# Kernel optimization log

Hardware: AMD Instinct MI355X
Metric: run time of the kernel (lower is better)

Reference implementation:

```python
import jax, jax.numpy as jnp
import numpy as np

B, N, K, EMB, OUT = 16, 1024, 20, 1024, 40
EPS = 1e-5  # BatchNorm eps; eval mode with running_mean=0, running_var=1


def _bn(x, g, b):
    # inference-mode batchnorm (running_mean=0, running_var=1) over channel axis 1
    shp = [1] * x.ndim
    shp[1] = x.shape[1]
    inv = 1.0 / jnp.sqrt(1.0 + EPS)
    return x * inv * g.reshape(shp) + b.reshape(shp)


def _lrelu(v):
    return jnp.where(v >= 0, v, 0.2 * v)


def _knn(x, k):
    # x: (B, C, N) -> (B, N, k) indices of k nearest neighbours
    inner = -2.0 * jnp.einsum('bcn,bcm->bnm', x, x)
    xx = jnp.sum(x * x, axis=1)  # (B, N)
    pd = -xx[:, :, None] - inner - xx[:, None, :]  # negative squared distance
    return jax.lax.top_k(pd, k)[1]


def _graph_feature(x, k):
    # x: (B, C, N) -> (B, 2C, N, k) edge features [x_j - x_i, x_i]
    idx = _knn(x, k)                          # (B, N, k)
    xt = jnp.transpose(x, (0, 2, 1))          # (B, N, C)
    feat = jax.vmap(lambda pts, ind: pts[ind])(xt, idx)  # (B, N, k, C)
    ctr = xt[:, :, None, :]                   # (B, N, 1, C)
    out = jnp.concatenate([feat - ctr, jnp.broadcast_to(ctr, feat.shape)], axis=3)
    return jnp.transpose(out, (0, 3, 1, 2))   # (B, 2C, N, k)


def _local_frames(x, k):
    # x: (B, 3, N) -> (B, 6, N, k); eigh-based local frame + topk gather (no_grad in torch)
    B_, _, N_ = x.shape
    diff = jnp.transpose(x[:, :, None, :] - x[:, :, :, None], (0, 2, 1, 3))  # (B,N,3,N): y[b,i,c,j]=x[b,c,j]-x[b,c,i]
    cov = jnp.einsum('bncm,bndm->bncd', diff, diff)  # (B,N,3,3)
    _, vecs = jnp.linalg.eigh(cov)
    y = jnp.einsum('bndc,bndm->bncm', vecs, diff)    # eigvecs^T @ diff, (B,N,3,N)
    diag = jnp.transpose(jnp.diagonal(y, axis1=1, axis2=3), (0, 2, 1))  # (B,N,3) = y[b,n,:,n]
    y_sub = y - diag[:, :, :, None]
    red = jnp.sum(y_sub * y_sub, axis=2)             # (B,N,N)
    idx = jax.lax.top_k(red, k)[1]                   # (B,N,k) largest
    idxe = jnp.broadcast_to(idx[:, :, None, :], (B_, N_, 3, k))
    gy = jnp.take_along_axis(y, idxe, axis=3)
    gs = jnp.take_along_axis(y_sub, idxe, axis=3)
    x0 = jnp.concatenate([gy, gs], axis=2)           # (B,N,6,k)
    return jnp.transpose(x0, (0, 2, 1, 3))           # (B,6,N,k)


def setup_inputs() -> dict:
    key = jax.random.key(0)
    ks = jax.random.split(key, 30)
    rn = lambda k_, s, sc=0.05: jax.random.normal(k_, s, jnp.float32) * sc
    gm = lambda k_, c: 1.0 + 0.1 * jax.random.normal(k_, (c,), jnp.float32)
    bt = lambda k_, c: 0.1 * jax.random.normal(k_, (c,), jnp.float32)
    return {
        'x': jax.random.normal(ks[0], (B, 3, N), jnp.float32),
        'w1': rn(ks[1], (64, 6)),    'g1': gm(ks[2], 64),  'b1': bt(ks[3], 64),
        'w2': rn(ks[4], (64, 128)),  'g2': gm(ks[5], 64),  'b2': bt(ks[6], 64),
        'w3': rn(ks[7], (128, 128)), 'g3': gm(ks[8], 128), 'b3': bt(ks[9], 128),
        'w4': rn(ks[10], (256, 256)),'g4': gm(ks[11], 256),'b4': bt(ks[12], 256),
        'w5': rn(ks[13], (EMB, 512)),'g5': gm(ks[14], EMB),'b5': bt(ks[15], EMB),
        'lw1': rn(ks[16], (512, 2 * EMB)), 'g6': gm(ks[17], 512), 'b6': bt(ks[18], 512),
        'lw2': rn(ks[19], (256, 512)), 'lb2': bt(ks[20], 256), 'g7': gm(ks[21], 256), 'b7': bt(ks[22], 256),
        'lw3': rn(ks[23], (OUT, 256)), 'lb3': bt(ks[24], OUT),
    }


def reference(x, w1, g1, b1, w2, g2, b2, w3, g3, b3, w4, g4, b4,
              w5, g5, b5, lw1, g6, b6, lw2, lb2, g7, b7, lw3, lb3):
    x0 = jax.lax.stop_gradient(_local_frames(x, K))      # torch.no_grad block
    h = _lrelu(_bn(jnp.einsum('oc,bcnk->bonk', w1, x0), g1, b1))
    x1 = jnp.max(h, axis=-1)                              # (B,64,N)
    h = _lrelu(_bn(jnp.einsum('oc,bcnk->bonk', w2, _graph_feature(x1, K)), g2, b2))
    x2 = jnp.max(h, axis=-1)                              # (B,64,N)
    h = _lrelu(_bn(jnp.einsum('oc,bcnk->bonk', w3, _graph_feature(x2, K)), g3, b3))
    x3 = jnp.max(h, axis=-1)                              # (B,128,N)
    h = _lrelu(_bn(jnp.einsum('oc,bcnk->bonk', w4, _graph_feature(x3, K)), g4, b4))
    x4 = jnp.max(h, axis=-1)                              # (B,256,N)
    xc = jnp.concatenate([x1, x2, x3, x4], axis=1)        # (B,512,N)
    h5 = _lrelu(_bn(jnp.einsum('oc,bcn->bon', w5, xc), g5, b5))  # (B,EMB,N)
    f = jnp.concatenate([jnp.max(h5, axis=-1), jnp.mean(h5, axis=-1)], axis=1)  # (B,2*EMB)
    f = _lrelu(_bn(f @ lw1.T, g6, b6))                    # dropout = identity (eval)
    f = _lrelu(_bn(f @ lw2.T + lb2, g7, b7))
    return f @ lw3.T + lb3                                # (B,OUT)
```

## Files before the change

kernel.cpp:

```cpp
#include <hip/hip_runtime.h>
#include <hip/hip_bf16.h>
#include <math.h>

#define BB 16
#define NN 1024
#define KK 20


__device__ inline float s_sign(float a, float b) { return b >= 0.0f ? fabsf(a) : -fabsf(a); }

__device__ inline float s_lapy2(float x, float y) {
    float xa = fabsf(x), ya = fabsf(y);
    float w = fmaxf(xa, ya), z = fminf(xa, ya);
    if (z == 0.0f) return w;
    float t = z / w;
    return w * sqrtf(1.0f + t * t);
}

__device__ inline void s_lartg(float f, float g, float& c, float& s, float& r) {
    const float safmin = 1.1754943508222875e-38f;
    const float safmax = 1.0f / 1.1754943508222875e-38f;
    const float rtmin = 1.0842021724855044e-19f;
    const float rtmax = 9.2233720368547758e+18f;
    float f1 = fabsf(f), g1 = fabsf(g);
    if (g == 0.0f) { c = 1.0f; s = 0.0f; r = f; }
    else if (f == 0.0f) { c = 0.0f; s = (g >= 0.0f ? 1.0f : -1.0f); r = g1; }
    else {
        float d;
        if (f1 > rtmin && f1 < rtmax && g1 > rtmin && g1 < rtmax) {
            d = sqrtf(f * f + g * g);
            c = f1 / d;
            r = (f >= 0.0f ? d : -d);
        } else {
            float u = fminf(safmax, fmaxf(safmin, fmaxf(f1, g1)));
            float fs = f / u, gs = g / u;
            d = sqrtf(fs * fs + gs * gs);
            c = fabsf(fs) / d;
            r = (f >= 0.0f ? d : -d);
            r = r * u;
        }
        s = g / r;
    }
}

__device__ void s_laev2(float a, float b, float cc, float& rt1, float& rt2,
                        float& cs1, float& sn1) {
    float sm = a + cc;
    float df = a - cc;
    float adf = fabsf(df);
    float tb = b + b;
    float ab = fabsf(tb);
    float acmx, acmn;
    if (fabsf(a) > fabsf(cc)) { acmx = a; acmn = cc; } else { acmx = cc; acmn = a; }
    float rt;
    if (adf > ab) { float t = ab / adf; rt = adf * sqrtf(1.0f + t * t); }
    else if (adf < ab) { float t = adf / ab; rt = ab * sqrtf(1.0f + t * t); }
    else rt = ab * sqrtf(2.0f);
    int sgn1;
    if (sm < 0.0f) { rt1 = 0.5f * (sm - rt); sgn1 = -1; rt2 = (acmx / rt1) * acmn - (b / rt1) * b; }
    else if (sm > 0.0f) { rt1 = 0.5f * (sm + rt); sgn1 = 1; rt2 = (acmx / rt1) * acmn - (b / rt1) * b; }
    else { rt1 = 0.5f * rt; rt2 = -0.5f * rt; sgn1 = 1; }
    float cs; int sgn2;
    if (df >= 0.0f) { cs = df + rt; sgn2 = 1; } else { cs = df - rt; sgn2 = -1; }
    float acs = fabsf(cs);
    if (acs > ab) {
        float ct = -tb / cs;
        sn1 = 1.0f / sqrtf(1.0f + ct * ct);
        cs1 = ct * sn1;
    } else {
        if (ab == 0.0f) { cs1 = 1.0f; sn1 = 0.0f; }
        else {
            float tn = -cs / tb;
            cs1 = 1.0f / sqrtf(1.0f + tn * tn);
            sn1 = tn * cs1;
        }
    }
    if (sgn1 == sgn2) { float tn = cs1; cs1 = -sn1; sn1 = tn; }
}

__device__ void ssteqr3(float* d, float* e, float z[4][4]) {
    const float EPS = 5.9604644775390625e-08f;
    const float EPS2 = 3.5527136788005009e-15f;
    const float SAFMIN = 1.1754943508222875e-38f;
    const float SAFMAX = 1.0f / 1.1754943508222875e-38f;
    const float SSFMAX = sqrtf(SAFMAX) / 3.0f;
    const float SSFMIN = sqrtf(SAFMIN) / EPS2;
    const int n = 3;
    float cwork[4], swork[4];
    int nmaxit = n * 30, jtot = 0;
    int l1 = 1, nm1 = n - 1;
    int l, lsv, lend, lendsv, m, iscale;
    float anorm = 0.0f, p, g, r, c, s, f, b, rt1, rt2;
    int i, j, mm;
    float tst, sc, temp, ct, st;

L10:
    if (l1 > n) goto L160;
    if (l1 > 1) e[l1 - 1] = 0.0f;
    if (l1 <= nm1) {
        for (m = l1; m <= nm1; ++m) {
            tst = fabsf(e[m]);
            if (tst == 0.0f) goto L30;
            if (tst <= (sqrtf(fabsf(d[m])) * sqrtf(fabsf(d[m + 1]))) * EPS) { e[m] = 0.0f; goto L30; }
        }
    }
    m = n;
L30:
    l = l1; lsv = l; lend = m; lendsv = lend; l1 = m + 1;
    if (lend == l) goto L10;
    anorm = 0.0f;
    for (i = l; i <= lend; ++i) anorm = fmaxf(anorm, fabsf(d[i]));
    for (i = l; i <= lend - 1; ++i) anorm = fmaxf(anorm, fabsf(e[i]));
    iscale = 0;
    if (anorm == 0.0f) goto L10;
    if (anorm > SSFMAX) {
        iscale = 1; sc = SSFMAX / anorm;
        for (i = l; i <= lend; ++i) d[i] *= sc;
        for (i = l; i <= lend - 1; ++i) e[i] *= sc;
    } else if (anorm < SSFMIN) {
        iscale = 2; sc = SSFMIN / anorm;
        for (i = l; i <= lend; ++i) d[i] *= sc;
        for (i = l; i <= lend - 1; ++i) e[i] *= sc;
    }
    if (fabsf(d[lend]) < fabsf(d[l])) { lend = lsv; l = lendsv; }
    if (lend > l) {
L40:
        if (l != lend) {
            for (m = l; m <= lend - 1; ++m) {
                tst = fabsf(e[m]); tst = tst * tst;
                if (tst <= (EPS2 * fabsf(d[m])) * fabsf(d[m + 1]) + SAFMIN) goto L60;
            }
        }
        m = lend;
L60:
        if (m < lend) e[m] = 0.0f;
        p = d[l];
        if (m == l) goto L80;
        if (m == l + 1) {
            s_laev2(d[l], e[l], d[l + 1], rt1, rt2, c, s);
            for (i = 1; i <= n; ++i) {
                temp = z[i][l + 1];
                z[i][l + 1] = c * temp - s * z[i][l];
                z[i][l] = s * temp + c * z[i][l];
            }
            d[l] = rt1; d[l + 1] = rt2; e[l] = 0.0f;
            l += 2;
            if (l <= lend) goto L40;
            goto L140;
        }
        if (jtot == nmaxit) goto L140;
        ++jtot;
        g = (d[l + 1] - p) / (2.0f * e[l]);
        r = s_lapy2(g, 1.0f);
        g = d[m] - p + (e[l] / (g + s_sign(r, g)));
        s = 1.0f; c = 1.0f; p = 0.0f;
        for (i = m - 1; i >= l; --i) {
            f = s * e[i]; b = c * e[i];
            s_lartg(g, f, c, s, r);
            if (i != m - 1) e[i + 1] = r;
            g = d[i + 1] - p;
            r = (d[i] - g) * s + 2.0f * c * b;
            p = s * r;
            d[i + 1] = g + p;
            g = c * r - b;
            cwork[i] = c; swork[i] = -s;
        }
        mm = m - l + 1;
        for (j = mm - 1; j >= 1; --j) {
            ct = cwork[l + j - 1]; st = swork[l + j - 1];
            for (i = 1; i <= n; ++i) {
                temp = z[i][l + j];
                z[i][l + j] = ct * temp - st * z[i][l + j - 1];
                z[i][l + j - 1] = st * temp + ct * z[i][l + j - 1];
            }
        }
        d[l] = d[l] - p;
        e[l] = g;
        goto L40;
L80:
        d[l] = p;
        l = l + 1;
        if (l <= lend) goto L40;
        goto L140;
    } else {
L90:
        if (l != lend) {
            for (m = l; m >= lend + 1; --m) {
                tst = fabsf(e[m - 1]); tst = tst * tst;
                if (tst <= (EPS2 * fabsf(d[m])) * fabsf(d[m - 1]) + SAFMIN) goto L110;
            }
        }
        m = lend;
L110:
    if (m > lend) e[m - 1] = 0.0f;
        p = d[l];
        if (m == l) goto L130;
        if (m == l - 1) {
            s_laev2(d[l - 1], e[l - 1], d[l], rt1, rt2, c, s);
            for (i = 1; i <= n; ++i) {
                temp = z[i][l];
                z[i][l] = c * temp - s * z[i][l - 1];
                z[i][l - 1] = s * temp + c * z[i][l - 1];
            }
            d[l - 1] = rt1; d[l] = rt2; e[l - 1] = 0.0f;
            l -= 2;
            if (l >= lend) goto L90;
            goto L140;
        }
        if (jtot == nmaxit) goto L140;
        ++jtot;
        g = (d[l - 1] - p) / (2.0f * e[l - 1]);
        r = s_lapy2(g, 1.0f);
        g = d[m] - p + (e[l - 1] / (g + s_sign(r, g)));
        s = 1.0f; c = 1.0f; p = 0.0f;
        for (i = m; i <= l - 1; ++i) {
            f = s * e[i]; b = c * e[i];
            s_lartg(g, f, c, s, r);
            if (i != m) e[i - 1] = r;
            g = d[i] - p;
            r = (d[i + 1] - g) * s + 2.0f * c * b;
            p = s * r;
            d[i] = g + p;
            g = c * r - b;
            cwork[i] = c; swork[i] = s;
        }
        mm = l - m + 1;
        for (j = 1; j <= mm - 1; ++j) {
            ct = cwork[m + j - 1]; st = swork[m + j - 1];
            for (i = 1; i <= n; ++i) {
                temp = z[i][m + j];
                z[i][m + j] = ct * temp - st * z[i][m + j - 1];
                z[i][m + j - 1] = st * temp + ct * z[i][m + j - 1];
            }
        }
        d[l] = d[l] - p;
        e[l - 1] = g;
        goto L90;
L130:
        d[l] = p;
        l = l - 1;
        if (l >= lend) goto L90;
        goto L140;
    }
L140:
    if (iscale == 1) {
        sc = anorm / SSFMAX;
        for (i = lsv; i <= lendsv; ++i) d[i] *= sc;
        for (i = lsv; i <= lendsv - 1; ++i) e[i] *= sc;
    } else if (iscale == 2) {
        sc = anorm / SSFMIN;
        for (i = lsv; i <= lendsv; ++i) d[i] *= sc;
        for (i = lsv; i <= lendsv - 1; ++i) e[i] *= sc;
    }
    if (jtot < nmaxit) goto L10;
    return;
L160:
    for (int ii = 2; ii <= n; ++ii) {
        i = ii - 1; int k = i;
        p = d[i];
        for (j = ii; j <= n; ++j) {
            if (d[j] < p) { k = j; p = d[j]; }
        }
        if (k != i) {
            d[k] = d[i]; d[i] = p;
            for (int rr = 1; rr <= n; ++rr) { float t = z[rr][i]; z[rr][i] = z[rr][k]; z[rr][k] = t; }
        }
    }
}

__device__ void eigh3f(const float A[3][3], float vecs[3][3]) {
    float a00 = A[0][0], a10 = A[1][0], a20 = A[2][0];
    float a11 = A[1][1], a21 = A[2][1], a22 = A[2][2];
    float d[4], e[4], tau1, v2 = 0.0f, beta;
    float alpha = a10, xnorm = fabsf(a20);
    if (xnorm == 0.0f) {
        tau1 = 0.0f; beta = alpha;
    } else {
        beta = -s_sign(s_lapy2(alpha, xnorm), alpha);
        tau1 = (beta - alpha) / beta;
        v2 = a20 * (1.0f / (alpha - beta));
    }
    e[1] = beta;
    if (tau1 != 0.0f) {
        float w0 = tau1 * (a11 + a21 * v2);
        float w1 = tau1 * (a21 + a22 * v2);
        float al = -0.5f * tau1 * (w0 + w1 * v2);
        w0 += al; w1 += al * v2;
        a11 = a11 - w0 - w0;
        a21 = a21 - v2 * w0 - w1;
        a22 = a22 - v2 * w1 - w1 * v2;
    }
    e[2] = a21;
    d[1] = a00; d[2] = a11; d[3] = a22;
    float z[4][4];
    for (int i = 1; i <= 3; ++i)
        for (int j = 1; j <= 3; ++j) z[i][j] = (i == j) ? 1.0f : 0.0f;
    ssteqr3(d, e, z);
    if (tau1 != 0.0f) {
        for (int j = 1; j <= 3; ++j) {
            float sum = z[2][j] + v2 * z[3][j];
            z[2][j] -= tau1 * sum;
            z[3][j] -= tau1 * v2 * sum;
        }
    }
    for (int c = 0; c < 3; ++c) {
        vecs[0][c] = z[1][c + 1];
        vecs[1][c] = z[2][c + 1];
        vecs[2][c] = z[3][c + 1];
    }
}

__global__ __launch_bounds__(256) void transpose_w2_kernel(const float* __restrict__ w,
                                                           float* __restrict__ wp,
                                                           int R, int C) {
    int i = blockIdx.x * 256 + threadIdx.x;
    if (i < R * C) {
        int r = i / C, c = i % C;
        int pc = c >> 1, k = c & 1;
        wp[((size_t)pc * R + r) * 2 + k] = w[i];
    }
}

__global__ __launch_bounds__(256) void transpose_w4_kernel(const float* __restrict__ w,
                                                           float* __restrict__ wq,
                                                           int R, int C) {
    int i = blockIdx.x * 256 + threadIdx.x;
    if (i < R * C) {
        int r = i / C, c = i % C;
        int qc = c >> 2, k = c & 3;
        wq[((size_t)qc * R + r) * 4 + k] = w[i];
    }
}

__global__ __launch_bounds__(256) void transpose_w_kernel(const float* __restrict__ w,
                                                          float* __restrict__ wt,
                                                          int R, int C) {
    int i = blockIdx.x * 256 + threadIdx.x;
    if (i < R * C) {
        int r = i / C, c = i % C;
        wt[(size_t)c * R + r] = w[i];
    }
}

template <int C>
__global__ __launch_bounds__(256) void transpose_x_kernel(const double* __restrict__ xt,
                                                          double* __restrict__ xtc) {
    __shared__ double tile[32][33];
    const int ctiles = C / 32, ntiles = NN / 32;
    int id = blockIdx.x;
    int b = id / (ctiles * ntiles);
    int rem = id % (ctiles * ntiles);
    int ct = rem / ntiles, nt = rem % ntiles;
    int c0 = ct * 32, n0 = nt * 32;
    int tc = threadIdx.x & 31, tr = threadIdx.x >> 5;
    for (int rr = tr; rr < 32; rr += 8)
        tile[rr][tc] = xt[((size_t)b * NN + n0 + rr) * C + c0 + tc];
    __syncthreads();
    for (int rr = tr; rr < 32; rr += 8)
        xtc[((size_t)b * C + c0 + rr) * NN + n0 + tc] = tile[tc][rr];
}

__global__ __launch_bounds__(256) void cov6_kernel(const float* __restrict__ x,
                                                   double* __restrict__ cov6) {
    int bn = blockIdx.x;
    int b = bn >> 10, n = bn & 1023;
    __shared__ double covp[6][4];
    const float* xb = x + (size_t)b * 3 * NN;
    float cx = xb[n], cy = xb[NN + n], cz = xb[2 * NN + n];
    double c00 = 0, c01 = 0, c02 = 0, c11 = 0, c12 = 0, c22 = 0;
    for (int m = threadIdx.x; m < NN; m += 256) {
        double dx = (double)xb[m] - (double)cx;
        double dy = (double)xb[NN + m] - (double)cy;
        double dz = (double)xb[2 * NN + m] - (double)cz;
        c00 += dx * dx; c01 += dx * dy; c02 += dx * dz;
        c11 += dy * dy; c12 += dy * dz; c22 += dz * dz;
    }
    for (int off = 32; off; off >>= 1) {
        c00 += __shfl_down(c00, off); c01 += __shfl_down(c01, off);
        c02 += __shfl_down(c02, off); c11 += __shfl_down(c11, off);
        c12 += __shfl_down(c12, off); c22 += __shfl_down(c22, off);
    }
    int lane = threadIdx.x & 63, wv = threadIdx.x >> 6;
    if (lane == 0) {
        covp[0][wv] = c00; covp[1][wv] = c01; covp[2][wv] = c02;
        covp[3][wv] = c11; covp[4][wv] = c12; covp[5][wv] = c22;
    }
    __syncthreads();
    if (threadIdx.x == 0) {
        double* outp = cov6 + (size_t)bn * 6;
        outp[0] = covp[0][0] + covp[0][1] + covp[0][2] + covp[0][3];
        outp[1] = covp[1][0] + covp[1][1] + covp[1][2] + covp[1][3];
        outp[2] = covp[2][0] + covp[2][1] + covp[2][2] + covp[2][3];
        outp[3] = covp[3][0] + covp[3][1] + covp[3][2] + covp[3][3];
        outp[4] = covp[4][0] + covp[4][1] + covp[4][2] + covp[4][3];
        outp[5] = covp[5][0] + covp[5][1] + covp[5][2] + covp[5][3];
    }
}

__global__ __launch_bounds__(256) void eigh_kernel(const double* __restrict__ cov6,
                                                   double* __restrict__ vecsg) {
    int i = blockIdx.x * 256 + threadIdx.x;
    if (i < BB * NN) {
        const double* s = cov6 + (size_t)i * 6;
        double s00 = s[0], s01 = s[1], s02 = s[2], s11 = s[3], s12 = s[4], s22 = s[5];
        float A[3][3];
        A[0][0] = (float)s00; A[0][1] = (float)s01; A[0][2] = (float)s02;
        A[1][0] = (float)s01; A[1][1] = (float)s11; A[1][2] = (float)s12;
        A[2][0] = (float)s02; A[2][1] = (float)s12; A[2][2] = (float)s22;
        float V[3][3];
        eigh3f(A, V);
        double* vp = vecsg + (size_t)i * 9;
        for (int dd = 0; dd < 3; ++dd)
            for (int cc2 = 0; cc2 < 3; ++cc2) vp[dd * 3 + cc2] = (double)V[dd][cc2];
    }
}

__global__ __launch_bounds__(256) void lf_rest_kernel(
    const float* __restrict__ x, const double* __restrict__ vecsg,
    const float* __restrict__ w1, const float* __restrict__ g1, const float* __restrict__ b1,
    float* __restrict__ x1, double* __restrict__ x1t) {
    int bn = blockIdx.x;
    int b = bn >> 10, n = bn & 1023;
    __shared__ float xs[3][NN];
    __shared__ double red[NN];
    __shared__ int sel[KK];
    __shared__ double ysel[3][KK];

    const float* xb = x + (size_t)b * 3 * NN;
    for (int t = threadIdx.x; t < 3 * NN; t += 256) xs[t >> 10][t & 1023] = xb[t];
    __syncthreads();

    float cx = xs[0][n], cy = xs[1][n], cz = xs[2][n];
    const double* vp = vecsg + (size_t)bn * 9;
    double v00 = vp[0], v01 = vp[1], v02 = vp[2];
    double v10 = vp[3], v11 = vp[4], v12 = vp[5];
    double v20 = vp[6], v21 = vp[7], v22 = vp[8];
    for (int m = threadIdx.x; m < NN; m += 256) {
        double dx = (double)xs[0][m] - (double)cx;
        double dy = (double)xs[1][m] - (double)cy;
        double dz = (double)xs[2][m] - (double)cz;
        double y0 = v00 * dx + v10 * dy + v20 * dz;
        double y1 = v01 * dx + v11 * dy + v21 * dz;
        double y2 = v02 * dx + v12 * dy + v22 * dz;
        red[m] = y0 * y0 + y1 * y1 + y2 * y2;
    }
    __syncthreads();
    if (threadIdx.x < 64) {
        double v[16];
#pragma unroll
        for (int j = 0; j < 16; ++j) v[j] = red[threadIdx.x + 64 * j];
        for (int it = 0; it < KK; ++it) {
            double bv = v[0]; int bj = 0;
#pragma unroll
            for (int j = 1; j < 16; ++j) {
                if (v[j] > bv) { bv = v[j]; bj = j; }
            }
            int bm = (bj << 6) + threadIdx.x;
            for (int off2 = 1; off2 < 64; off2 <<= 1) {
                double ov = __shfl_xor(bv, off2);
                int om = __shfl_xor(bm, off2);
                if (ov > bv || (ov == bv && om < bm)) { bv = ov; bm = om; }
            }
            int cj = bm >> 6;
            bool mine = (bm & 63) == (int)threadIdx.x;
#pragma unroll
            for (int j = 0; j < 16; ++j)
                if (j == cj && mine) v[j] = -1.0;
            if (threadIdx.x == 0) sel[it] = bm;
        }
    }
    __syncthreads();
    if (threadIdx.x < KK) {
        int m = sel[threadIdx.x];
        double dx = (double)xs[0][m] - (double)cx;
        double dy = (double)xs[1][m] - (double)cy;
        double dz = (double)xs[2][m] - (double)cz;
        ysel[0][threadIdx.x] = v00 * dx + v10 * dy + v20 * dz;
        ysel[1][threadIdx.x] = v01 * dx + v11 * dy + v21 * dz;
        ysel[2][threadIdx.x] = v02 * dx + v12 * dy + v22 * dz;
    }
    __syncthreads();
    if (threadIdx.x < 64) {
        int o = threadIdx.x;
        double wr0 = w1[o * 6 + 0], wr1 = w1[o * 6 + 1], wr2 = w1[o * 6 + 2];
        double wr3 = w1[o * 6 + 3], wr4 = w1[o * 6 + 4], wr5 = w1[o * 6 + 5];
        const double inv = 1.0 / sqrt(1.0 + 1e-5);
        double go = g1[o], bo = b1[o];
        double best = -INFINITY;
        for (int j = 0; j < KK; ++j) {
            double y0 = ysel[0][j], y1 = ysel[1][j], y2 = ysel[2][j];
            double a = wr0 * y0 + wr1 * y1 + wr2 * y2 + wr3 * y0 + wr4 * y1 + wr5 * y2;
            double h = a * inv * go + bo;
            h = h >= 0.0 ? h : 0.2 * h;
            best = fmax(best, h);
        }
        x1[((size_t)b * 64 + o) * NN + n] = (float)best;
        x1t[((size_t)(b * NN + n)) * 64 + o] = best;
    }
}

template <int C>
__global__ __launch_bounds__(256) void xx_kernel(const double* __restrict__ xtc, double* __restrict__ xx) {
    int i = blockIdx.x * 256 + threadIdx.x;
    if (i < BB * NN) {
        int b = i >> 10, m = i & 1023;
        const double* col = xtc + (size_t)b * C * NN + m;
        double s = 0.0;
        for (int c = 0; c < C; ++c) s = fma(col[(size_t)c * NN], col[(size_t)c * NN], s);
        xx[i] = s;
    }
}

template <int C>
__global__ __launch_bounds__(512) void knn_kernel(const double* __restrict__ xt,
                                                  const double* __restrict__ xtc,
                                                  const double* __restrict__ xx,
                                                  int* __restrict__ idx) {
    int b = blockIdx.x >> 7;
    int n0 = (blockIdx.x & 127) << 3;
    __shared__ alignas(16) double ctr[8][C];
    __shared__ alignas(16) double pdh[8][512];
    __shared__ double xxqs[8];
    int tid = threadIdx.x;

    const double* qbase = xt + (size_t)(b * NN + n0) * C;
    for (int t = tid; t < 8 * C; t += 512) (&ctr[0][0])[t] = qbase[t];
    if (tid < 8) xxqs[tid] = xx[b * NN + n0 + tid];
    __syncthreads();

    int wv = tid >> 6, lane = tid & 63;
    double v[16];
    const double* colb = xtc + (size_t)b * C * NN;

    for (int h = 0; h < 2; ++h) {
        int m = h * 512 + tid;
        double acc[8];
#pragma unroll
        for (int q = 0; q < 8; ++q) acc[q] = 0.0;
#pragma unroll 4
        for (int c = 0; c < C; ++c) {
            double rv = colb[(size_t)c * NN + m];
            double c0 = ctr[0][c], c1 = ctr[1][c], c2 = ctr[2][c], c3 = ctr[3][c];
            double c4 = ctr[4][c], c5 = ctr[5][c], c6 = ctr[6][c], c7 = ctr[7][c];
            acc[0] = fma(c0, rv, acc[0]);
            acc[1] = fma(c1, rv, acc[1]);
            acc[2] = fma(c2, rv, acc[2]);
            acc[3] = fma(c3, rv, acc[3]);
            acc[4] = fma(c4, rv, acc[4]);
            acc[5] = fma(c5, rv, acc[5]);
            acc[6] = fma(c6, rv, acc[6]);
            acc[7] = fma(c7, rv, acc[7]);
        }
        double xm = xx[b * NN + m];
        if (h == 1) __syncthreads();
#pragma unroll
        for (int q = 0; q < 8; ++q)
            pdh[q][tid] = (-xxqs[q] + 2.0 * acc[q]) - xm;
        __syncthreads();
#pragma unroll
        for (int j = 0; j < 8; ++j) v[8 * h + j] = pdh[wv][lane + 64 * j];
    }

    int* out = idx + (size_t)(b * NN + n0 + wv) * KK;
    for (int it = 0; it < KK; ++it) {
        double bv = v[0]; int bj = 0;
#pragma unroll
        for (int j = 1; j < 16; ++j) {
            if (v[j] > bv) { bv = v[j]; bj = j; }
        }
        int bm = (bj << 6) + lane;
        for (int off = 1; off < 64; off <<= 1) {
            double ov = __shfl_xor(bv, off);
            int om = __shfl_xor(bm, off);
            if (ov > bv || (ov == bv && om < bm)) { bv = ov; bm = om; }
        }
        int cj = bm >> 6;
        bool mine = (bm & 63) == lane;
#pragma unroll
        for (int j = 0; j < 16; ++j)
            if (j == cj && mine) v[j] = -INFINITY;
        if (lane == 0) out[it] = bm;
    }
}

template <int CIN, int COUT, int P>
__global__ __launch_bounds__(256) void conv_kernel(
    const double* __restrict__ xint, const int* __restrict__ idx,
    const float* __restrict__ wp, const float* __restrict__ g, const float* __restrict__ bbias,
    float* __restrict__ xout, double* __restrict__ xoutt) {
    const int bpb = NN / P;
    int b = blockIdx.x / bpb;
    int n0 = (blockIdx.x % bpb) * P;
    int tid = threadIdx.x;
    int o = tid % COUT, p = tid / COUT;
    int n = n0 + p;

    __shared__ alignas(16) double ctr[P][CIN];
    __shared__ alignas(16) double dif[P][KK][CIN];
    __shared__ int midx[P][KK];

    const double* qbase = xint + (size_t)(b * NN + n0) * CIN;
    for (int t = tid; t < P * CIN; t += 256) (&ctr[0][0])[t] = qbase[t];
    for (int t = tid; t < P * KK; t += 256)
        (&midx[0][0])[t] = idx[(size_t)(b * NN + n0 + t / KK) * KK + (t % KK)];
    __syncthreads();
    for (int t = tid; t < P * KK * CIN; t += 256) {
        int p2 = t / (KK * CIN);
        int rem = t % (KK * CIN);
        int j = rem / CIN, c = rem % CIN;
        dif[p2][j][c] = xint[(size_t)(b * NN + midx[p2][j]) * CIN + c] - ctr[p2][c];
    }
    __syncthreads();

    const double inv = 1.0 / sqrt(1.0 + 1e-5);
    const float2* wpo = reinterpret_cast<const float2*>(wp) + o;
    double ct2 = 0.0;
#pragma unroll 4
    for (int c2 = 0; c2 < CIN / 2; ++c2) {
        float2 wv = wpo[(size_t)(CIN / 2 + c2) * COUT];
        double2 cv = *reinterpret_cast<const double2*>(&ctr[p][2 * c2]);
        ct2 = fma((double)wv.x, cv.x, ct2);
        ct2 = fma((double)wv.y, cv.y, ct2);
    }
    double acc[KK];
#pragma unroll
    for (int j = 0; j < KK; ++j) acc[j] = 0.0;
    for (int c2 = 0; c2 < CIN / 2; ++c2) {
        float2 wv = wpo[(size_t)c2 * COUT];
        double wx = (double)wv.x, wy = (double)wv.y;
#pragma unroll
        for (int j = 0; j < KK; ++j) {
            double2 dv = *reinterpret_cast<const double2*>(&dif[p][j][2 * c2]);
            acc[j] = fma(wx, dv.x, acc[j]);
            acc[j] = fma(wy, dv.y, acc[j]);
        }
    }
    double go = g[o], bo = bbias[o];
    double best = -INFINITY;
#pragma unroll
    for (int j = 0; j < KK; ++j) {
        double h = (acc[j] + ct2) * inv * go + bo;
        h = h >= 0.0 ? h : 0.2 * h;
        best = fmax(best, h);
    }
    xout[((size_t)b * COUT + o) * NN + n] = (float)best;
    if (xoutt) xoutt[(size_t)(b * NN + n) * COUT + o] = best;
}

__global__ __launch_bounds__(256) void gemm_ab4_kernel(
    const double* __restrict__ x3t, const float* __restrict__ wq,
    float* __restrict__ AB) {
    int b = blockIdx.x >> 8;
    int n0 = (blockIdx.x & 255) << 2;
    int o = threadIdx.x;
    __shared__ alignas(16) float xr[4][128];
    for (int t = threadIdx.x; t < 4 * 128; t += 256)
        xr[t >> 7][t & 127] = (float)x3t[((size_t)(b * NN + n0 + (t >> 7))) * 128 + (t & 127)];
    __syncthreads();
    const float4* wqc = reinterpret_cast<const float4*>(wq) + o;
    float accA[4], accB[4];
#pragma unroll
    for (int p = 0; p < 4; ++p) { accA[p] = 0.f; accB[p] = 0.f; }
    for (int qc = 0; qc < 32; ++qc) {
        float4 wv = wqc[(size_t)qc * 256];
#pragma unroll
        for (int p = 0; p < 4; ++p) {
            float4 xv = *reinterpret_cast<const float4*>(&xr[p][4 * qc]);
            accA[p] = fmaf(wv.x, xv.x, accA[p]); accA[p] = fmaf(wv.y, xv.y, accA[p]);
            accA[p] = fmaf(wv.z, xv.z, accA[p]); accA[p] = fmaf(wv.w, xv.w, accA[p]);
        }
    }
    for (int qc = 32; qc < 64; ++qc) {
        float4 wv = wqc[(size_t)qc * 256];
#pragma unroll
        for (int p = 0; p < 4; ++p) {
            float4 xv = *reinterpret_cast<const float4*>(&xr[p][4 * (qc - 32)]);
            accB[p] = fmaf(wv.x, xv.x, accB[p]); accB[p] = fmaf(wv.y, xv.y, accB[p]);
            accB[p] = fmaf(wv.z, xv.z, accB[p]); accB[p] = fmaf(wv.w, xv.w, accB[p]);
        }
    }
#pragma unroll
    for (int p = 0; p < 4; ++p) {
        float* row = AB + ((size_t)(b * NN + n0 + p)) * 512;
        row[o] = accA[p];
        row[256 + o] = accB[p];
    }
}

__global__ __launch_bounds__(256) void epi4_kernel(
    const float* __restrict__ AB, const int* __restrict__ idx,
    const float* __restrict__ g, const float* __restrict__ bbias,
    float* __restrict__ x4b) {
    int b = blockIdx.x >> 8;
    int n0 = (blockIdx.x & 255) << 2;
    int o = threadIdx.x;
    __shared__ int midx[4][KK];
    for (int t = threadIdx.x; t < 4 * KK; t += 256)
        midx[t / KK][t % KK] = idx[(size_t)(b * NN + n0 + t / KK) * KK + (t % KK)];
    __syncthreads();
    const float inv = (float)(1.0 / sqrt(1.0 + 1e-5));
    float s = inv * g[o];
    float bo = bbias[o];
#pragma unroll
    for (int p = 0; p < 4; ++p) {
        const float* ABn = AB + ((size_t)(b * NN + n0 + p)) * 512;
        float base = ABn[256 + o] - ABn[o];
        float best = -INFINITY;
        for (int j = 0; j < KK; ++j) {
            float aj = AB[((size_t)(b * NN + midx[p][j])) * 512 + o];
            float h = fmaf(aj + base, s, bo);
            h = h >= 0.f ? h : 0.2f * h;
            best = fmaxf(best, h);
        }
        x4b[((size_t)b * 256 + o) * NN + n0 + p] = best;
    }
}

__global__ __launch_bounds__(256) void gemm5_kernel(
    const float* __restrict__ x1, const float* __restrict__ x2,
    const float* __restrict__ x3, const float* __restrict__ x4,
    const float* __restrict__ w5t, const float* __restrict__ g5, const float* __restrict__ b5,
    float* __restrict__ pmax, float* __restrict__ psum) {
    int ot = blockIdx.x, nt = blockIdx.y, b = blockIdx.z;
    int o0 = ot * 128, n0 = nt * 128;
    __shared__ alignas(16) float Wt[16][132];
    __shared__ alignas(16) float Xt[16][132];
    __shared__ float rmax[128][17];
    __shared__ float rsum[128][17];
    float acc[8][8];
#pragma unroll
    for (int i = 0; i < 8; ++i)
#pragma unroll
        for (int j = 0; j < 8; ++j) acc[i][j] = 0.f;
    int tx = threadIdx.x & 15;
    int ty = threadIdx.x >> 4;
    int ka = threadIdx.x >> 5;
    int qa = threadIdx.x & 31;

    float4 wreg0, wreg1, xreg0, xreg1;

    {
        wreg0 = *reinterpret_cast<const float4*>(&w5t[(size_t)(ka)*1024 + o0 + 4 * qa]);
        wreg1 = *reinterpret_cast<const float4*>(&w5t[(size_t)(ka + 8) * 1024 + o0 + 4 * qa]);
#pragma unroll
        for (int r = 0; r < 2; ++r) {
            int c = ka + 8 * r;
            const float* src; int coff, CC;
            if (c < 64) { src = x1; coff = c; CC = 64; }
            else { src = x2; coff = c - 64; CC = 64; }
            float4 v = *reinterpret_cast<const float4*>(&src[((size_t)b * CC + coff) * NN + n0 + 4 * qa]);
            if (r == 0) xreg0 = v; else xreg1 = v;
        }
        *reinterpret_cast<float4*>(&Wt[ka][4 * qa]) = wreg0;
        *reinterpret_cast<float4*>(&Wt[ka + 8][4 * qa]) = wreg1;
        *reinterpret_cast<float4*>(&Xt[ka][4 * qa]) = xreg0;
        *reinterpret_cast<float4*>(&Xt[ka + 8][4 * qa]) = xreg1;
    }
    __syncthreads();

    for (int kk = 0; kk < 512; kk += 16) {
        bool more = (kk + 16) < 512;
        if (more) {
            int kk2 = kk + 16;
            wreg0 = *reinterpret_cast<const float4*>(&w5t[(size_t)(kk2 + ka) * 1024 + o0 + 4 * qa]);
            wreg1 = *reinterpret_cast<const float4*>(&w5t[(size_t)(kk2 + ka + 8) * 1024 + o0 + 4 * qa]);
#pragma unroll
            for (int r = 0; r < 2; ++r) {
                int c = kk2 + ka + 8 * r;
                const float* src; int coff, CC;
                if (c < 64) { src = x1; coff = c; CC = 64; }
                else if (c < 128) { src = x2; coff = c - 64; CC = 64; }
                else if (c < 256) { src = x3; coff = c - 128; CC = 128; }
                else { src = x4; coff = c - 256; CC = 256; }
                float4 v = *reinterpret_cast<const float4*>(&src[((size_t)b * CC + coff) * NN + n0 + 4 * qa]);
                if (r == 0) xreg0 = v; else xreg1 = v;
            }
        }
#pragma unroll
        for (int k = 0; k < 16; ++k) {
            float4 w0 = *reinterpret_cast<const float4*>(&Wt[k][ty * 4]);
            float4 w1 = *reinterpret_cast<const float4*>(&Wt[k][64 + ty * 4]);
            float4 xa = *reinterpret_cast<const float4*>(&Xt[k][tx * 4]);
            float4 xb2 = *reinterpret_cast<const float4*>(&Xt[k][64 + tx * 4]);
            float wv[8] = {w0.x, w0.y, w0.z, w0.w, w1.x, w1.y, w1.z, w1.w};
            float xv[8] = {xa.x, xa.y, xa.z, xa.w, xb2.x, xb2.y, xb2.z, xb2.w};
#pragma unroll
            for (int i = 0; i < 8; ++i)
#pragma unroll
                for (int j = 0; j < 8; ++j) acc[i][j] += wv[i] * xv[j];
        }
        __syncthreads();
        if (more) {
            *reinterpret_cast<float4*>(&Wt[ka][4 * qa]) = wreg0;
            *reinterpret_cast<float4*>(&Wt[ka + 8][4 * qa]) = wreg1;
            *reinterpret_cast<float4*>(&Xt[ka][4 * qa]) = xreg0;
            *reinterpret_cast<float4*>(&Xt[ka + 8][4 * qa]) = xreg1;
            __syncthreads();
        }
    }
    const float inv = (float)(1.0 / sqrt(1.0 + 1e-5));
#pragma unroll
    for (int i = 0; i < 8; ++i) {
        int o = (i < 4) ? (ty * 4 + i) : (64 + ty * 4 + (i - 4));
        float go = g5[o0 + o], bo = b5[o0 + o];
        float mx = -INFINITY, sm = 0.f;
#pragma unroll
        for (int j = 0; j < 8; ++j) {
            float h = acc[i][j] * inv * go + bo;
            h = h >= 0.f ? h : 0.2f * h;
            mx = fmaxf(mx, h);
            sm += h;
        }
        rmax[o][tx] = mx; rsum[o][tx] = sm;
    }
    __syncthreads();
    if (threadIdx.x < 128) {
        int o = threadIdx.x;
        float mx = -INFINITY, sm = 0.f;
        for (int t = 0; t < 16; ++t) { mx = fmaxf(mx, rmax[o][t]); sm += rsum[o][t]; }
        pmax[((size_t)b * 1024 + o0 + o) * 16 + nt] = mx;
        psum[((size_t)b * 1024 + o0 + o) * 16 + nt] = sm;
    }
}

__global__ __launch_bounds__(256) void poolfc_kernel(
    const float* __restrict__ pmax, const float* __restrict__ psum,
    const float* __restrict__ lw1, const float* __restrict__ g6, const float* __restrict__ b6,
    const float* __restrict__ lw2, const float* __restrict__ lb2,
    const float* __restrict__ g7, const float* __restrict__ b7,
    const float* __restrict__ lw3, const float* __restrict__ lb3,
    float* __restrict__ out) {
    int b = blockIdx.x;
    __shared__ float f[2048];
    __shared__ float f2[512];
    __shared__ float f3[256];
    for (int o = threadIdx.x; o < 1024; o += 256) {
        float mx = -INFINITY, sm = 0.f;
        for (int t = 0; t < 8; ++t) {
            mx = fmaxf(mx, pmax[((size_t)b * 1024 + o) * 16 + t]);
            sm += psum[((size_t)b * 1024 + o) * 16 + t];
        }
        f[o] = mx;
        f[1024 + o] = sm * (1.0f / 1024.0f);
    }
    __syncthreads();
    const float inv = (float)(1.0 / sqrt(1.0 + 1e-5));
    for (int o = threadIdx.x; o < 512; o += 256) {
        const float* wr = lw1 + (size_t)o * 2048;
        float acc = 0.f;
        for (int c = 0; c < 2048; ++c) acc += wr[c] * f[c];
        float h = acc * inv * g6[o] + b6[o];
        f2[o] = h >= 0.f ? h : 0.2f * h;
    }
    __syncthreads();
    for (int o = threadIdx.x; o < 256; o += 256) {
        const float* wr = lw2 + (size_t)o * 512;
        float acc = 0.f;
        for (int c = 0; c < 512; ++c) acc += wr[c] * f2[c];
        acc += lb2[o];
        float h = acc * inv * g7[o] + b7[o];
        f3[o] = h >= 0.f ? h : 0.2f * h;
    }
    __syncthreads();
    if (threadIdx.x < 40) {
        int o = threadIdx.x;
        const float* wr = lw3 + (size_t)o * 256;
        float acc = 0.f;
        for (int c = 0; c < 256; ++c) acc += wr[c] * f3[c];
        out[b * 40 + o] = acc + lb3[o];
    }
}

extern "C" void kernel_launch(void* const* d_in, const int* in_sizes, int n_in,
                              void* d_out, int out_size, void* d_ws, size_t ws_size,
                              hipStream_t stream) {
    const float* x   = (const float*)d_in[0];
    const float* w1  = (const float*)d_in[1];
    const float* g1  = (const float*)d_in[2];
    const float* b1  = (const float*)d_in[3];
    const float* w2  = (const float*)d_in[4];
    const float* g2  = (const float*)d_in[5];
    const float* b2  = (const float*)d_in[6];
    const float* w3  = (const float*)d_in[7];
    const float* g3  = (const float*)d_in[8];
    const float* b3  = (const float*)d_in[9];
    const float* w4  = (const float*)d_in[10];
    const float* g4  = (const float*)d_in[11];
    const float* b4  = (const float*)d_in[12];
    const float* w5  = (const float*)d_in[13];
    const float* g5  = (const float*)d_in[14];
    const float* b5  = (const float*)d_in[15];
    const float* lw1 = (const float*)d_in[16];
    const float* g6  = (const float*)d_in[17];
    const float* b6  = (const float*)d_in[18];
    const float* lw2 = (const float*)d_in[19];
    const float* lb2 = (const float*)d_in[20];
    const float* g7  = (const float*)d_in[21];
    const float* b7  = (const float*)d_in[22];
    const float* lw3 = (const float*)d_in[23];
    const float* lb3 = (const float*)d_in[24];

    float* ws = (float*)d_ws;
    size_t off = 0;
    float* x1b  = ws + off; off += (size_t)BB * 64 * NN;
    float* x2b  = ws + off; off += (size_t)BB * 64 * NN;
    float* x3b  = ws + off; off += (size_t)BB * 128 * NN;
    float* x4b  = ws + off; off += (size_t)BB * 256 * NN;
    float* pmax = ws + off; off += (size_t)BB * 1024 * 16;
    float* psum = ws + off; off += (size_t)BB * 1024 * 16;
    int*   idxb = (int*)(ws + off); off += (size_t)BB * NN * KK;
    float* w2t  = ws + off; off += (size_t)64 * 128;
    float* w3t  = ws + off; off += (size_t)128 * 128;
    float* w4t  = ws + off; off += (size_t)256 * 256;
    float* w5t  = ws + off; off += (size_t)512 * 1024;
    float* ab4  = ws + off; off += (size_t)BB * NN * 512;
    off = (off + 3) & ~(size_t)3;
    double* x1t = (double*)(ws + off); off += (size_t)BB * NN * 64 * 2;
    double* x2t = (double*)(ws + off); off += (size_t)BB * NN * 64 * 2;
    double* x3t = (double*)(ws + off); off += (size_t)BB * NN * 128 * 2;
    double* x1c = (double*)(ws + off); off += (size_t)BB * 64 * NN * 2;
    double* x2c = (double*)(ws + off); off += (size_t)BB * 64 * NN * 2;
    double* x3c = (double*)(ws + off); off += (size_t)BB * 128 * NN * 2;
    double* xxd = (double*)(ws + off); off += (size_t)BB * NN * 2;
    double* cov6g = (double*)(ws + off); off += (size_t)BB * NN * 6 * 2;
    double* vecsg = (double*)(ws + off); off += (size_t)BB * NN * 9 * 2;

    dim3 blk(256);
    dim3 blk512(512);
    transpose_w2_kernel<<<dim3((64 * 128 + 255) / 256), blk, 0, stream>>>(w2, w2t, 64, 128);
    transpose_w2_kernel<<<dim3((128 * 128 + 255) / 256), blk, 0, stream>>>(w3, w3t, 128, 128);
    transpose_w4_kernel<<<dim3((256 * 256 + 255) / 256), blk, 0, stream>>>(w4, w4t, 256, 256);
    transpose_w_kernel<<<dim3((1024 * 512 + 255) / 256), blk, 0, stream>>>(w5, w5t, 1024, 512);

    cov6_kernel<<<dim3(BB * NN), blk, 0, stream>>>(x, cov6g);
    eigh_kernel<<<dim3(BB * NN / 256), blk, 0, stream>>>(cov6g, vecsg);
    lf_rest_kernel<<<dim3(BB * NN), blk, 0, stream>>>(x, vecsg, w1, g1, b1, x1b, x1t);

    transpose_x_kernel<64><<<dim3(BB * 2 * 32), blk, 0, stream>>>(x1t, x1c);
    xx_kernel<64><<<dim3(BB * NN / 256), blk, 0, stream>>>(x1c, xxd);
    knn_kernel<64><<<dim3(BB * NN / 8), blk512, 0, stream>>>(x1t, x1c, xxd, idxb);
    conv_kernel<64, 64, 4><<<dim3(BB * NN / 4), blk, 0, stream>>>(x1t, idxb, w2t, g2, b2, x2b, x2t);
    transpose_x_kernel<64><<<dim3(BB * 2 * 32), blk, 0, stream>>>(x2t, x2c);
    xx_kernel<64><<<dim3(BB * NN / 256), blk, 0, stream>>>(x2c, xxd);
    knn_kernel<64><<<dim3(BB * NN / 8), blk512, 0, stream>>>(x2t, x2c, xxd, idxb);
    conv_kernel<64, 128, 2><<<dim3(BB * NN / 2), blk, 0, stream>>>(x2t, idxb, w3t, g3, b3, x3b, x3t);
    transpose_x_kernel<128><<<dim3(BB * 4 * 32), blk, 0, stream>>>(x3t, x3c);
    xx_kernel<128><<<dim3(BB * NN / 256), blk, 0, stream>>>(x3c, xxd);
    knn_kernel<128><<<dim3(BB * NN / 8), blk512, 0, stream>>>(x3t, x3c, xxd, idxb);
    gemm_ab4_kernel<<<dim3(BB * NN / 4), blk, 0, stream>>>(x3t, w4t, ab4);
    epi4_kernel<<<dim3(BB * NN / 4), blk, 0, stream>>>(ab4, idxb, g4, b4, x4b);
    gemm5_kernel<<<dim3(8, 8, BB), blk, 0, stream>>>(x1b, x2b, x3b, x4b, w5t, g5, b5, pmax, psum);
    poolfc_kernel<<<dim3(BB), blk, 0, stream>>>(pmax, psum, lw1, g6, b6, lw2, lb2, g7, b7, lw3, lb3,
                                                (float*)d_out);
}
```

Baseline: 1.751 ms.

## Process eight query points per block in local-frame top-k kernel

The local-frame kernel now handles 8 points per 512-thread block instead of one point per 256-thread block. The shared x tile is loaded once per 8 queries, and each wavefront runs the top-k selection for its own query, so all waves do useful work where before only one did. This reduces redundant global loads and idle threads. It costs more shared memory per block (about 32KB of doubles) and a two-pass staging step with extra barriers.

```diff
diff --git a/kernel.cpp b/kernel.cpp
--- a/kernel.cpp
+++ b/kernel.cpp
@@ -415,80 +415,92 @@
     }
 }
 
-__global__ __launch_bounds__(256) void lf_rest_kernel(
+__global__ __launch_bounds__(512) void lf_rest_kernel(
     const float* __restrict__ x, const double* __restrict__ vecsg,
     const float* __restrict__ w1, const float* __restrict__ g1, const float* __restrict__ b1,
     float* __restrict__ x1, double* __restrict__ x1t) {
-    int bn = blockIdx.x;
-    int b = bn >> 10, n = bn & 1023;
+    int b = blockIdx.x >> 7;
+    int n0 = (blockIdx.x & 127) << 3;
+    int tid = threadIdx.x;
+    int wv = tid >> 6, lane = tid & 63;
+
     __shared__ float xs[3][NN];
-    __shared__ double red[NN];
-    __shared__ int sel[KK];
-    __shared__ double ysel[3][KK];
+    __shared__ double red8[8][512];
+    __shared__ double vq[8][9];
+    __shared__ float ctrq[8][3];
+    __shared__ int sel8[8][KK];
+    __shared__ double ysel8[8][3][KK];
 
     const float* xb = x + (size_t)b * 3 * NN;
-    for (int t = threadIdx.x; t < 3 * NN; t += 256) xs[t >> 10][t & 1023] = xb[t];
-    __syncthreads();
-
-    float cx = xs[0][n], cy = xs[1][n], cz = xs[2][n];
-    const double* vp = vecsg + (size_t)bn * 9;
-    double v00 = vp[0], v01 = vp[1], v02 = vp[2];
-    double v10 = vp[3], v11 = vp[4], v12 = vp[5];
-    double v20 = vp[6], v21 = vp[7], v22 = vp[8];
-    for (int m = threadIdx.x; m < NN; m += 256) {
-        double dx = (double)xs[0][m] - (double)cx;
-        double dy = (double)xs[1][m] - (double)cy;
-        double dz = (double)xs[2][m] - (double)cz;
-        double y0 = v00 * dx + v10 * dy + v20 * dz;
-        double y1 = v01 * dx + v11 * dy + v21 * dz;
-        double y2 = v02 * dx + v12 * dy + v22 * dz;
-        red[m] = y0 * y0 + y1 * y1 + y2 * y2;
-    }
-    __syncthreads();
-    if (threadIdx.x < 64) {
-        double v[16];
-#pragma unroll
-        for (int j = 0; j < 16; ++j) v[j] = red[threadIdx.x + 64 * j];
-        for (int it = 0; it < KK; ++it) {
-            double bv = v[0]; int bj = 0;
-#pragma unroll
-            for (int j = 1; j < 16; ++j) {
-                if (v[j] > bv) { bv = v[j]; bj = j; }
-            }
-            int bm = (bj << 6) + threadIdx.x;
-            for (int off2 = 1; off2 < 64; off2 <<= 1) {
-                double ov = __shfl_xor(bv, off2);
-                int om = __shfl_xor(bm, off2);
-                if (ov > bv || (ov == bv && om < bm)) { bv = ov; bm = om; }
-            }
-            int cj = bm >> 6;
-            bool mine = (bm & 63) == (int)threadIdx.x;
-#pragma unroll
-            for (int j = 0; j < 16; ++j)
-                if (j == cj && mine) v[j] = -1.0;
-            if (threadIdx.x == 0) sel[it] = bm;
-        }
-    }
-    __syncthreads();
-    if (threadIdx.x < KK) {
-        int m = sel[threadIdx.x];
-        double dx = (double)xs[0][m] - (double)cx;
-        double dy = (double)xs[1][m] - (double)cy;
-        double dz = (double)xs[2][m] - (double)cz;
-        ysel[0][threadIdx.x] = v00 * dx + v10 * dy + v20 * dz;
-        ysel[1][threadIdx.x] = v01 * dx + v11 * dy + v21 * dz;
-        ysel[2][threadIdx.x] = v02 * dx + v12 * dy + v22 * dz;
-    }
-    __syncthreads();
-    if (threadIdx.x < 64) {
-        int o = threadIdx.x;
+    for (int t = tid; t < 3 * NN; t += 512) xs[t >> 10][t & 1023] = xb[t];
+    if (tid < 72) vq[tid / 9][tid % 9] = vecsg[((size_t)(b * NN + n0 + tid / 9)) * 9 + tid % 9];
+    if (tid < 24) ctrq[tid / 3][tid % 3] = xb[(tid % 3) * NN + n0 + tid / 3];
+    __syncthreads();
+
+    double v[16];
+    for (int h = 0; h < 2; ++h) {
+        int m = h * 512 + tid;
+        float xm0 = xs[0][m], xm1 = xs[1][m], xm2 = xs[2][m];
+        double racc[8];
+#pragma unroll
+        for (int q = 0; q < 8; ++q) {
+            double dx = (double)xm0 - (double)ctrq[q][0];
+            double dy = (double)xm1 - (double)ctrq[q][1];
+            double dz = (double)xm2 - (double)ctrq[q][2];
+            double y0 = vq[q][0] * dx + vq[q][3] * dy + vq[q][6] * dz;
+            double y1 = vq[q][1] * dx + vq[q][4] * dy + vq[q][7] * dz;
+            double y2 = vq[q][2] * dx + vq[q][5] * dy + vq[q][8] * dz;
+            racc[q] = y0 * y0 + y1 * y1 + y2 * y2;
+        }
+        if (h == 1) __syncthreads();
+#pragma unroll
+        for (int q = 0; q < 8; ++q) red8[q][tid] = racc[q];
+        __syncthreads();
+#pragma unroll
+        for (int j = 0; j < 8; ++j) v[8 * h + j] = red8[wv][lane + 64 * j];
+    }
+
+    for (int it = 0; it < KK; ++it) {
+        double bv = v[0]; int bj = 0;
+#pragma unroll
+        for (int j = 1; j < 16; ++j) {
+            if (v[j] > bv) { bv = v[j]; bj = j; }
+        }
+        int bm = (bj << 6) + lane;
+        for (int off2 = 1; off2 < 64; off2 <<= 1) {
+            double ov = __shfl_xor(bv, off2);
+            int om = __shfl_xor(bm, off2);
+            if (ov > bv || (ov == bv && om < bm)) { bv = ov; bm = om; }
+        }
+        int cj = bm >> 6;
+        bool mine = (bm & 63) == lane;
+#pragma unroll
+        for (int j = 0; j < 16; ++j)
+            if (j == cj && mine) v[j] = -1.0;
+        if (lane == 0) sel8[wv][it] = bm;
+    }
+    __syncthreads();
+
+    if (lane < KK) {
+        int m = sel8[wv][lane];
+        double dx = (double)xs[0][m] - (double)ctrq[wv][0];
+        double dy = (double)xs[1][m] - (double)ctrq[wv][1];
+        double dz = (double)xs[2][m] - (double)ctrq[wv][2];
+        ysel8[wv][0][lane] = vq[wv][0] * dx + vq[wv][3] * dy + vq[wv][6] * dz;
+        ysel8[wv][1][lane] = vq[wv][1] * dx + vq[wv][4] * dy + vq[wv][7] * dz;
+        ysel8[wv][2][lane] = vq[wv][2] * dx + vq[wv][5] * dy + vq[wv][8] * dz;
+    }
+    __syncthreads();
+
+    {
+        int o = lane, q = wv, n = n0 + q;
         double wr0 = w1[o * 6 + 0], wr1 = w1[o * 6 + 1], wr2 = w1[o * 6 + 2];
         double wr3 = w1[o * 6 + 3], wr4 = w1[o * 6 + 4], wr5 = w1[o * 6 + 5];
         const double inv = 1.0 / sqrt(1.0 + 1e-5);
         double go = g1[o], bo = b1[o];
         double best = -INFINITY;
         for (int j = 0; j < KK; ++j) {
-            double y0 = ysel[0][j], y1 = ysel[1][j], y2 = ysel[2][j];
+            double y0 = ysel8[q][0][j], y1 = ysel8[q][1][j], y2 = ysel8[q][2][j];
             double a = wr0 * y0 + wr1 * y1 + wr2 * y2 + wr3 * y0 + wr4 * y1 + wr5 * y2;
             double h = a * inv * go + bo;
             h = h >= 0.0 ? h : 0.2 * h;
@@ -934,7 +946,7 @@
 
     cov6_kernel<<<dim3(BB * NN), blk, 0, stream>>>(x, cov6g);
     eigh_kernel<<<dim3(BB * NN / 256), blk, 0, stream>>>(cov6g, vecsg);
-    lf_rest_kernel<<<dim3(BB * NN), blk, 0, stream>>>(x, vecsg, w1, g1, b1, x1b, x1t);
+    lf_rest_kernel<<<dim3(BB * NN / 8), blk512, 0, stream>>>(x, vecsg, w1, g1, b1, x1b, x1t);
 
     transpose_x_kernel<64><<<dim3(BB * 2 * 32), blk, 0, stream>>>(x1t, x1c);
     xx_kernel<64><<<dim3(BB * NN / 256), blk, 0, stream>>>(x1c, xxd);
```

New measurement: 1.607 ms. 8.2% less time.
